# Kernel optimization log

Measured on AMD Instinct MI355X. Metric: run time of the kernel, lower is better.

## Reference

```python
import jax, jax.numpy as jnp
import numpy as np

B, S, D, H = 2, 2048, 1024, 16  # batch, seq, rep_dim, num_heads
DH = D // H
MASK_VALUE = -1e-06  # value passed by MHAttention to masked_softmax (NOT -1e6)


def setup_inputs() -> dict:
    key = jax.random.key(0)
    ks = jax.random.split(key, 16)
    def xavier(k, shape):
        fan_in, fan_out = shape[0], shape[1]
        limit = float(np.sqrt(6.0 / (fan_in + fan_out)))
        return jax.random.uniform(k, shape, jnp.float32, -limit, limit)
    return {
        "queries": jax.random.normal(ks[0], (B, S, D), jnp.float32),
        "keys": jax.random.normal(ks[1], (B, S, D), jnp.float32),
        "values": jax.random.normal(ks[2], (B, S, D), jnp.float32),
        "thresholds": jax.random.randint(ks[3], (B,), 1, S + 1, jnp.int32),
        # Linear params stored as (in, out) so y = x @ W + b
        "Wq": xavier(ks[4], (D, D)), "bq": jnp.zeros((D,), jnp.float32),
        "Wk": xavier(ks[5], (D, D)), "bk": jnp.zeros((D,), jnp.float32),
        "Wv": xavier(ks[6], (D, D)), "bv": jnp.zeros((D,), jnp.float32),
        "W": xavier(ks[7], (DH, DH)),  # learnable bilinear attention matrix
        "Wo": xavier(ks[8], (D, D)), "bo": jnp.zeros((D,), jnp.float32),
    }


def reference(queries, keys, values, thresholds, Wq, bq, Wk, bk, Wv, bv, W, Wo, bo):
    def split_heads(x):  # (B,S,D) -> (B,H,S,DH)
        return x.reshape(B, S, H, DH).transpose(0, 2, 1, 3)

    Q = split_heads(queries @ Wq + bq)
    K = split_heads(keys @ Wk + bk)
    V = split_heads(values @ Wv + bv)

    # bilinear scores: (Q @ W) @ K^T, no 1/sqrt(d) scaling in original
    scores = jnp.einsum("bhqd,bhkd->bhqk", Q @ W, K)
    # mask key positions >= threshold[b] with MASK_VALUE before softmax
    keep = jnp.arange(S)[None, None, None, :] < thresholds[:, None, None, None]
    scores = jnp.where(keep, scores, MASK_VALUE)
    attn = jax.nn.softmax(scores, axis=-1)

    out = jnp.einsum("bhqk,bhkd->bhqd", attn, V)
    out = out.transpose(0, 2, 1, 3).reshape(B, S, D)  # merge heads
    return out @ Wo + bo
```

## Files before the change

### kernel.cpp

```cpp
#include <hip/hip_runtime.h>
#include <hip/hip_bf16.h>

#define D_MODEL 1024
#define NHEADS  16
#define DH      64
#define SEQ     2048
#define BATCH   2

#define LOG2E 1.4426950408889634f
#define MASKB2 (-1e-6f * LOG2E)
#define DEFER_THR 11.5456f
#define NEG_INF (-__builtin_inff())

typedef __attribute__((ext_vector_type(8))) short short8;
typedef __attribute__((ext_vector_type(4))) short short4v;
typedef __attribute__((ext_vector_type(4))) float f32x4;

#define AS1C(p) ((const __attribute__((address_space(1))) void*)(p))
#define AS3(p)  ((__attribute__((address_space(3))) void*)(p))

union PB { short4v s4; unsigned int u[2]; };

static __device__ __forceinline__ float fexp2(float x) {
    return __builtin_amdgcn_exp2f(x);
}

static __device__ __forceinline__ unsigned int pk2(float lo, float hi) {
    __hip_bfloat16 a = __float2bfloat16(lo), b = __float2bfloat16(hi);
    unsigned short au = *(unsigned short*)&a, bu = *(unsigned short*)&b;
    return (unsigned int)au | ((unsigned int)bu << 16);
}

__global__ __launch_bounds__(256) void fold_kernel(const float* __restrict__ Wq,
                                                   const float* __restrict__ bq,
                                                   const float* __restrict__ W,
                                                   float* __restrict__ Wq2,
                                                   float* __restrict__ bq2) {
    if (blockIdx.x < 4096) {
        int idx = blockIdx.x * 256 + threadIdx.x;
        int row = idx >> 10;
        int col = idx & 1023;
        int h = col >> 6, j = col & 63;
        const float* wqr = Wq + (size_t)row * D_MODEL + h * DH;
        float s = 0.f;
#pragma unroll
        for (int d = 0; d < DH; ++d) s += wqr[d] * W[d * DH + j];
        Wq2[idx] = s * LOG2E;
    } else {
        int col = (blockIdx.x - 4096) * 256 + threadIdx.x;
        int h = col >> 6, j = col & 63;
        float s = 0.f;
#pragma unroll
        for (int d = 0; d < DH; ++d) s += bq[h * DH + d] * W[d * DH + j];
        bq2[col] = s * LOG2E;
    }
}

__global__ __launch_bounds__(256) void convert3_kernel(const float* __restrict__ q,
                                                       const float* __restrict__ k,
                                                       const float* __restrict__ v,
                                                       __hip_bfloat16* __restrict__ oq,
                                                       __hip_bfloat16* __restrict__ ok,
                                                       __hip_bfloat16* __restrict__ ov) {
    int z = blockIdx.x >> 11;
    int i = (blockIdx.x & 2047) * 256 + threadIdx.x;
    const float* in = (z == 0) ? q : (z == 1) ? k : v;
    __hip_bfloat16* out = (z == 0) ? oq : (z == 1) ? ok : ov;
    float4 a = *(const float4*)(in + (size_t)i * 8);
    float4 b = *(const float4*)(in + (size_t)i * 8 + 4);
    __hip_bfloat16 o[8];
    o[0] = __float2bfloat16(a.x); o[1] = __float2bfloat16(a.y);
    o[2] = __float2bfloat16(a.z); o[3] = __float2bfloat16(a.w);
    o[4] = __float2bfloat16(b.x); o[5] = __float2bfloat16(b.y);
    o[6] = __float2bfloat16(b.z); o[7] = __float2bfloat16(b.w);
    *(short8*)(out + (size_t)i * 8) = *(short8*)o;
}

__global__ __launch_bounds__(256) void transpose4_kernel(const float* __restrict__ W0,
                                                         const float* __restrict__ W1,
                                                         const float* __restrict__ W2,
                                                         const float* __restrict__ W3,
                                                         __hip_bfloat16* __restrict__ T0,
                                                         __hip_bfloat16* __restrict__ T1,
                                                         __hip_bfloat16* __restrict__ T2,
                                                         __hip_bfloat16* __restrict__ T3) {
    __shared__ float sT[32][33];
    int z = blockIdx.z;
    const float* Win = (z == 0) ? W0 : (z == 1) ? W1 : (z == 2) ? W2 : W3;
    __hip_bfloat16* Wt = (z == 0) ? T0 : (z == 1) ? T1 : (z == 2) ? T2 : T3;
    int n0 = blockIdx.x * 32, k0 = blockIdx.y * 32;
    int tx = threadIdx.x & 31, ty = threadIdx.x >> 5;
#pragma unroll
    for (int i = 0; i < 4; ++i)
        sT[ty + i * 8][tx] = Win[(size_t)(k0 + ty + i * 8) * D_MODEL + n0 + tx];
    __syncthreads();
#pragma unroll
    for (int i = 0; i < 4; ++i)
        Wt[(size_t)(n0 + ty + i * 8) * D_MODEL + k0 + tx] = __float2bfloat16(sT[tx][ty + i * 8]);
}

#define GEMM_CORE(A_, BT_)                                                                  \
    __shared__ __hip_bfloat16 sA[2][128 * 32];                                              \
    __shared__ __hip_bfloat16 sB[2][64 * 32];                                               \
    const int t = threadIdx.x;                                                              \
    const int lane = t & 63, w = t >> 6;                                                    \
    const int g = lane >> 4, li = lane & 15;                                                \
    const int r0 = blockIdx.y * 128, c0 = blockIdx.x * 64;                                  \
    const int wr = (w >> 1) * 64, wc = (w & 1) * 32;                                        \
    f32x4 acc[4][2] = {};                                                                   \
    auto stage = [&](int bb, int k0) {                                                      \
        _Pragma("unroll")                                                                   \
        for (int i = 0; i < 2; ++i) {                                                       \
            int o = (i * 4 + w) * 1024 + lane * 16;                                         \
            int row = o >> 6, ce = (o & 63) >> 1;                                           \
            __builtin_amdgcn_global_load_lds(AS1C(A_ + (size_t)(r0 + row) * 1024 + k0 + ce),\
                                             AS3((char*)sA[bb] + (i * 4 + w) * 1024), 16, 0, 0); \
        }                                                                                   \
        {                                                                                   \
            int o = w * 1024 + lane * 16;                                                   \
            int row = o >> 6, ce = (o & 63) >> 1;                                           \
            __builtin_amdgcn_global_load_lds(AS1C(BT_ + (size_t)(c0 + row) * 1024 + k0 + ce),\
                                             AS3((char*)sB[bb] + w * 1024), 16, 0, 0);      \
        }                                                                                   \
    };                                                                                      \
    stage(0, 0);                                                                            \
    asm volatile("s_waitcnt vmcnt(0)" ::: "memory");                                        \
    __syncthreads();                                                                        \
    int cur = 0;                                                                            \
    for (int k0 = 0; k0 < 1024; k0 += 32) {                                                 \
        if (k0 + 32 < 1024) stage(cur ^ 1, k0 + 32);                                        \
        short8 af[4], bf[2];                                                                \
        _Pragma("unroll")                                                                   \
        for (int m = 0; m < 4; ++m)                                                         \
            af[m] = *(const short8*)(sA[cur] + (wr + m * 16 + li) * 32 + g * 8);            \
        _Pragma("unroll")                                                                   \
        for (int n = 0; n < 2; ++n)                                                         \
            bf[n] = *(const short8*)(sB[cur] + (wc + n * 16 + li) * 32 + g * 8);            \
        _Pragma("unroll")                                                                   \
        for (int m = 0; m < 4; ++m)                                                         \
            _Pragma("unroll")                                                               \
            for (int n = 0; n < 2; ++n)                                                     \
                acc[m][n] = __builtin_amdgcn_mfma_f32_16x16x32_bf16(af[m], bf[n], acc[m][n], 0, 0, 0); \
        asm volatile("s_waitcnt vmcnt(0)" ::: "memory");                                    \
        __syncthreads();                                                                    \
        cur ^= 1;                                                                           \
    }

__global__ __launch_bounds__(256) void gemm_qkv_kernel(
    const __hip_bfloat16* __restrict__ Xq, const __hip_bfloat16* __restrict__ Xk,
    const __hip_bfloat16* __restrict__ Xv,
    const __hip_bfloat16* __restrict__ WqT, const __hip_bfloat16* __restrict__ WkT,
    const __hip_bfloat16* __restrict__ WvT,
    const float* __restrict__ bq2, const float* __restrict__ bk, const float* __restrict__ bv,
    __hip_bfloat16* __restrict__ Qp, __hip_bfloat16* __restrict__ Kp,
    __hip_bfloat16* __restrict__ Vt) {
    const int z = blockIdx.z;
    const __hip_bfloat16* A  = (z == 0) ? Xq  : (z == 1) ? Xk  : Xv;
    const __hip_bfloat16* BT = (z == 0) ? WqT : (z == 1) ? WkT : WvT;
    const float* bias        = (z == 0) ? bq2 : (z == 1) ? bk  : bv;
    __hip_bfloat16* C        = (z == 0) ? Qp  : (z == 1) ? Kp  : Vt;

    GEMM_CORE(A, BT)

#pragma unroll
    for (int m = 0; m < 4; ++m) {
#pragma unroll
        for (int n = 0; n < 2; ++n) {
            int col = c0 + wc + n * 16 + li;
            float bs = bias[col];
            int row0 = r0 + wr + m * 16 + g * 4;
            int h = col >> 6, d = col & 63;
            if (z == 2) {
                int b = row0 >> 11, s0 = row0 & 2047;
                __hip_bfloat16 o4[4];
#pragma unroll
                for (int r = 0; r < 4; ++r) o4[r] = __float2bfloat16(acc[m][n][r] + bs);
                *(short4*)(C + (((size_t)(b * NHEADS + h)) * DH + d) * SEQ + s0) = *(short4*)o4;
            } else {
#pragma unroll
                for (int r = 0; r < 4; ++r) {
                    int row = row0 + r;
                    int b = row >> 11, s = row & 2047;
                    C[(((size_t)(b * NHEADS + h)) * SEQ + s) * DH + d] =
                        __float2bfloat16(acc[m][n][r] + bs);
                }
            }
        }
    }
}

__global__ __launch_bounds__(256) void gemm_out_kernel(
    const __hip_bfloat16* __restrict__ A, const __hip_bfloat16* __restrict__ BT,
    const float* __restrict__ bias, float* __restrict__ C) {
    GEMM_CORE(A, BT)
#pragma unroll
    for (int m = 0; m < 4; ++m) {
#pragma unroll
        for (int n = 0; n < 2; ++n) {
            int col = c0 + wc + n * 16 + li;
            float bs = bias[col];
            int row0 = r0 + wr + m * 16 + g * 4;
#pragma unroll
            for (int r = 0; r < 4; ++r)
                C[(size_t)(row0 + r) * D_MODEL + col] = acc[m][n][r] + bs;
        }
    }
}

__global__ __launch_bounds__(256) void vsum_kernel(const __hip_bfloat16* __restrict__ Vt,
                                                   const int* __restrict__ thresholds,
                                                   float* __restrict__ Vsum) {
    int bh = blockIdx.x, b = bh >> 4;
    int thresh = thresholds[b];
    int loop_end = min(SEQ, ((thresh + 63) >> 6) << 6);
    int t = threadIdx.x;
    int dh = t >> 2, sub = t & 3;
    const __hip_bfloat16* row = Vt + ((size_t)bh * DH + dh) * SEQ;
    float s = 0.f;
    for (int s0 = loop_end + sub * 8; s0 < SEQ; s0 += 32) {
        short8 v = *(const short8*)(row + s0);
#pragma unroll
        for (int j = 0; j < 8; ++j) {
            unsigned short us = (unsigned short)v[j];
            s += __bfloat162float(*(__hip_bfloat16*)&us);
        }
    }
    s += __shfl_xor(s, 1);
    s += __shfl_xor(s, 2);
    if (sub == 0) Vsum[bh * DH + dh] = s;
}

__global__ __launch_bounds__(256) void attn_mfma_kernel(
    const __hip_bfloat16* __restrict__ Qp,
    const __hip_bfloat16* __restrict__ Kp,
    const __hip_bfloat16* __restrict__ Vt,
    const int* __restrict__ thresholds,
    const float* __restrict__ Vsum,
    __hip_bfloat16* __restrict__ AO) {
    __shared__ char lds[32768];
    char* sK  = lds;
    char* sVT = lds + 16384;

    const int t = threadIdx.x, lane = t & 63, w = t >> 6;
    const int g = lane >> 4, li = lane & 15;
    const int bh = blockIdx.x, b = bh >> 4, h = bh & 15;
    const int q0 = blockIdx.y * 128;
    const int thresh = thresholds[b];
    const int loop_end = min(SEQ, ((thresh + 63) >> 6) << 6);
    const __hip_bfloat16* Qb = Qp + (size_t)bh * SEQ * DH;
    const __hip_bfloat16* Kb = Kp + (size_t)bh * SEQ * DH;
    const __hip_bfloat16* Vb = Vt + (size_t)bh * DH * SEQ;

    short8 qf[2][2];
#pragma unroll
    for (int mq = 0; mq < 2; ++mq)
#pragma unroll
        for (int kb = 0; kb < 2; ++kb)
            qf[mq][kb] = *(const short8*)(Qb + (size_t)(q0 + w * 32 + mq * 16 + li) * DH +
                                          kb * 32 + g * 8);

    f32x4 Oacc[2][4] = {};
    float mrun[2] = {NEG_INF, NEG_INF};
    float lrun[2] = {0.f, 0.f};

    auto stageK = [&](int bb, int kv) {
#pragma unroll
        for (int i = 0; i < 2; ++i) {
            int o = i * 4096 + w * 1024 + lane * 16;
            int key = o >> 7, slot = (o & 127) >> 4;
            __builtin_amdgcn_global_load_lds(
                AS1C(Kb + (size_t)(kv + key) * DH + ((slot ^ (key & 7)) << 3)),
                AS3(sK + bb * 8192 + i * 4096 + w * 1024), 16, 0, 0);
        }
    };
    auto stageV = [&](int bb, int kv) {
#pragma unroll
        for (int i = 0; i < 2; ++i) {
            int o = i * 4096 + w * 1024 + lane * 16;
            int dh = o >> 7, slot = (o & 127) >> 4;
            __builtin_amdgcn_global_load_lds(
                AS1C(Vb + (size_t)dh * SEQ + kv + ((slot ^ (dh & 7)) << 3)),
                AS3(sVT + bb * 8192 + i * 4096 + w * 1024), 16, 0, 0);
        }
    };

    stageK(0, 0); stageV(0, 0);
    asm volatile("s_waitcnt vmcnt(0)" ::: "memory");
    __syncthreads();

    int cur = 0;
    for (int kv0 = 0; kv0 < loop_end; kv0 += 64) {
        int nxt = kv0 + 64;
        if (nxt < loop_end) { stageK(cur ^ 1, nxt); stageV(cur ^ 1, nxt); }

        f32x4 S[2][4] = {};
        __builtin_amdgcn_s_setprio(1);
#pragma unroll
        for (int kb = 0; kb < 2; ++kb) {
            short8 kf[4];
#pragma unroll
            for (int n = 0; n < 4; ++n) {
                int key = 16 * n + li;
                kf[n] = *(const short8*)(sK + cur * 8192 + key * 128 +
                                         (((4 * kb + g) ^ (key & 7)) << 4));
            }
#pragma unroll
            for (int mq = 0; mq < 2; ++mq)
#pragma unroll
                for (int n = 0; n < 4; ++n)
                    S[mq][n] = __builtin_amdgcn_mfma_f32_16x16x32_bf16(kf[n], qf[mq][kb],
                                                                       S[mq][n], 0, 0, 0);
        }
        __builtin_amdgcn_s_setprio(0);

        if (kv0 + 64 > thresh) {
            int tr = thresh - kv0 - 4 * g;
#pragma unroll
            for (int n = 0; n < 4; ++n)
#pragma unroll
                for (int rr = 0; rr < 4; ++rr)
                    if (16 * n + rr >= tr) { S[0][n][rr] = MASKB2; S[1][n][rr] = MASKB2; }
        }

        float pmax[2];
#pragma unroll
        for (int mq = 0; mq < 2; ++mq) {
            float mx = S[mq][0][0];
#pragma unroll
            for (int n = 0; n < 4; ++n)
#pragma unroll
                for (int rr = 0; rr < 4; ++rr) mx = fmaxf(mx, S[mq][n][rr]);
            mx = fmaxf(mx, __shfl_xor(mx, 16));
            mx = fmaxf(mx, __shfl_xor(mx, 32));
            pmax[mq] = mx;
        }

        bool need = (pmax[0] > mrun[0] + DEFER_THR) || (pmax[1] > mrun[1] + DEFER_THR);
        if (__any(need)) {
#pragma unroll
            for (int mq = 0; mq < 2; ++mq) {
                float mn = fmaxf(mrun[mq], pmax[mq]);
                float alpha = fexp2(mrun[mq] - mn);
                lrun[mq] *= alpha;
#pragma unroll
                for (int n = 0; n < 4; ++n)
#pragma unroll
                    for (int rr = 0; rr < 4; ++rr) Oacc[mq][n][rr] *= alpha;
                mrun[mq] = mn;
            }
        }

        short4v pb[2][4];
#pragma unroll
        for (int mq = 0; mq < 2; ++mq) {
            float rs = 0.f;
#pragma unroll
            for (int n = 0; n < 4; ++n) {
#pragma unroll
                for (int rr = 0; rr < 4; ++rr) {
                    float p = fexp2(S[mq][n][rr] - mrun[mq]);
                    S[mq][n][rr] = p;
                    rs += p;
                }
                PB u;
                u.u[0] = pk2(S[mq][n][0], S[mq][n][1]);
                u.u[1] = pk2(S[mq][n][2], S[mq][n][3]);
                pb[mq][n] = u.s4;
            }
            rs += __shfl_xor(rs, 16);
            rs += __shfl_xor(rs, 32);
            lrun[mq] += rs;
        }

        __builtin_amdgcn_s_setprio(1);
#pragma unroll
        for (int ks = 0; ks < 4; ++ks) {
            int slot = 2 * ks + (g >> 1);
            int sub8 = 8 * (g & 1);
#pragma unroll
            for (int n = 0; n < 4; ++n) {
                int dh = 16 * n + li;
                short4v va = *(const short4v*)(sVT + cur * 8192 + dh * 128 +
                                               ((slot ^ (dh & 7)) << 4) + sub8);
#pragma unroll
                for (int mq = 0; mq < 2; ++mq)
                    Oacc[mq][n] = __builtin_amdgcn_mfma_f32_16x16x16bf16_1k(va, pb[mq][ks],
                                                                            Oacc[mq][n], 0, 0, 0);
            }
        }
        __builtin_amdgcn_s_setprio(0);

        asm volatile("s_waitcnt vmcnt(0)" ::: "memory");
        __syncthreads();
        cur ^= 1;
    }

    int nmask = SEQ - loop_end;
    if (nmask > 0) {
        const float* vs = Vsum + bh * DH;
        f32x4 vsf[4];
#pragma unroll
        for (int n = 0; n < 4; ++n) vsf[n] = *(const f32x4*)(vs + 16 * n + 4 * g);
#pragma unroll
        for (int mq = 0; mq < 2; ++mq) {
            float pu = fexp2(MASKB2 - mrun[mq]);
            lrun[mq] += (float)nmask * pu;
#pragma unroll
            for (int n = 0; n < 4; ++n)
#pragma unroll
                for (int rr = 0; rr < 4; ++rr) Oacc[mq][n][rr] += pu * vsf[n][rr];
        }
    }

#pragma unroll
    for (int mq = 0; mq < 2; ++mq) {
        float linv = 1.0f / lrun[mq];
        int q = q0 + w * 32 + mq * 16 + li;
#pragma unroll
        for (int n = 0; n < 4; ++n) {
            __hip_bfloat16 o4[4];
#pragma unroll
            for (int rr = 0; rr < 4; ++rr) o4[rr] = __float2bfloat16(Oacc[mq][n][rr] * linv);
            *(short4*)(AO + (size_t)(b * SEQ + q) * D_MODEL + h * DH + 16 * n + 4 * g) =
                *(short4*)o4;
        }
    }
}

extern "C" void kernel_launch(void* const* d_in, const int* in_sizes, int n_in,
                              void* d_out, int out_size, void* d_ws, size_t ws_size,
                              hipStream_t stream) {
    const float* queries    = (const float*)d_in[0];
    const float* keys       = (const float*)d_in[1];
    const float* values     = (const float*)d_in[2];
    const int*   thresholds = (const int*)d_in[3];
    const float* Wq = (const float*)d_in[4];
    const float* bq = (const float*)d_in[5];
    const float* Wk = (const float*)d_in[6];
    const float* bk = (const float*)d_in[7];
    const float* Wv = (const float*)d_in[8];
    const float* bv = (const float*)d_in[9];
    const float* W  = (const float*)d_in[10];
    const float* Wo = (const float*)d_in[11];
    const float* bo = (const float*)d_in[12];
    float* out = (float*)d_out;

    char* wsb = (char*)d_ws;
    float* bq2  = (float*)wsb;
    float* Vsum = (float*)(wsb + 4096);
    float* Wq2  = (float*)(wsb + 16384);
    __hip_bfloat16* XqB = (__hip_bfloat16*)(wsb + 16384 + (4 << 20));
    __hip_bfloat16* XkB = XqB + (1 << 22);
    __hip_bfloat16* XvB = XkB + (1 << 22);
    __hip_bfloat16* WqT = XvB + (1 << 22);
    __hip_bfloat16* WkT = WqT + (1 << 20);
    __hip_bfloat16* WvT = WkT + (1 << 20);
    __hip_bfloat16* WoT = WvT + (1 << 20);
    __hip_bfloat16* QpB = WoT + (1 << 20);
    __hip_bfloat16* KpB = QpB + (1 << 22);
    __hip_bfloat16* VtB = KpB + (1 << 22);
    __hip_bfloat16* AOB = XqB;

    fold_kernel<<<4100, 256, 0, stream>>>(Wq, bq, W, Wq2, bq2);
    convert3_kernel<<<6144, 256, 0, stream>>>(queries, keys, values, XqB, XkB, XvB);
    transpose4_kernel<<<dim3(32, 32, 4), 256, 0, stream>>>(Wq2, Wk, Wv, Wo,
                                                           WqT, WkT, WvT, WoT);

    gemm_qkv_kernel<<<dim3(16, 32, 3), 256, 0, stream>>>(XqB, XkB, XvB, WqT, WkT, WvT,
                                                         bq2, bk, bv, QpB, KpB, VtB);
    vsum_kernel<<<32, 256, 0, stream>>>(VtB, thresholds, Vsum);

    attn_mfma_kernel<<<dim3(32, 16), 256, 0, stream>>>(QpB, KpB, VtB, thresholds, Vsum, AOB);

    gemm_out_kernel<<<dim3(16, 32), 256, 0, stream>>>(AOB, WoT, bo, out);
}
```

Baseline: 181.6 us.

## Drop LDS staging in attention; load K/V directly from global per wave

The attention kernel now runs one wave per block (64 threads, 2048 blocks) instead of four waves sharing double-buffered, swizzled K/V tiles in LDS. Each wave reads its K and V fragments straight from global memory, which removes the LDS staging, the barriers and the waitcnt syncs. The cost is that K/V reuse across the four waves now has to come from the L2/L1 cache, and the V reads are narrow 8-byte strided accesses. The row-max reduction is also rewritten as a balanced tree.

```diff
diff --git a/kernel.cpp b/kernel.cpp
--- a/kernel.cpp
+++ b/kernel.cpp
@@ -230,21 +230,17 @@
     if (sub == 0) Vsum[bh * DH + dh] = s;
 }
 
-__global__ __launch_bounds__(256) void attn_mfma_kernel(
+__global__ __launch_bounds__(64) void attn_mfma_kernel(
     const __hip_bfloat16* __restrict__ Qp,
     const __hip_bfloat16* __restrict__ Kp,
     const __hip_bfloat16* __restrict__ Vt,
     const int* __restrict__ thresholds,
     const float* __restrict__ Vsum,
     __hip_bfloat16* __restrict__ AO) {
-    __shared__ char lds[32768];
-    char* sK  = lds;
-    char* sVT = lds + 16384;
-
-    const int t = threadIdx.x, lane = t & 63, w = t >> 6;
+    const int lane = threadIdx.x;
     const int g = lane >> 4, li = lane & 15;
     const int bh = blockIdx.x, b = bh >> 4, h = bh & 15;
-    const int q0 = blockIdx.y * 128;
+    const int q0 = blockIdx.y * 32;
     const int thresh = thresholds[b];
     const int loop_end = min(SEQ, ((thresh + 63) >> 6) << 6);
     const __hip_bfloat16* Qb = Qp + (size_t)bh * SEQ * DH;
@@ -256,61 +252,32 @@
     for (int mq = 0; mq < 2; ++mq)
 #pragma unroll
         for (int kb = 0; kb < 2; ++kb)
-            qf[mq][kb] = *(const short8*)(Qb + (size_t)(q0 + w * 32 + mq * 16 + li) * DH +
+            qf[mq][kb] = *(const short8*)(Qb + (size_t)(q0 + mq * 16 + li) * DH +
                                           kb * 32 + g * 8);
 
     f32x4 Oacc[2][4] = {};
     float mrun[2] = {NEG_INF, NEG_INF};
     float lrun[2] = {0.f, 0.f};
 
-    auto stageK = [&](int bb, int kv) {
-#pragma unroll
-        for (int i = 0; i < 2; ++i) {
-            int o = i * 4096 + w * 1024 + lane * 16;
-            int key = o >> 7, slot = (o & 127) >> 4;
-            __builtin_amdgcn_global_load_lds(
-                AS1C(Kb + (size_t)(kv + key) * DH + ((slot ^ (key & 7)) << 3)),
-                AS3(sK + bb * 8192 + i * 4096 + w * 1024), 16, 0, 0);
-        }
-    };
-    auto stageV = [&](int bb, int kv) {
-#pragma unroll
-        for (int i = 0; i < 2; ++i) {
-            int o = i * 4096 + w * 1024 + lane * 16;
-            int dh = o >> 7, slot = (o & 127) >> 4;
-            __builtin_amdgcn_global_load_lds(
-                AS1C(Vb + (size_t)dh * SEQ + kv + ((slot ^ (dh & 7)) << 3)),
-                AS3(sVT + bb * 8192 + i * 4096 + w * 1024), 16, 0, 0);
-        }
-    };
-
-    stageK(0, 0); stageV(0, 0);
-    asm volatile("s_waitcnt vmcnt(0)" ::: "memory");
-    __syncthreads();
-
-    int cur = 0;
     for (int kv0 = 0; kv0 < loop_end; kv0 += 64) {
-        int nxt = kv0 + 64;
-        if (nxt < loop_end) { stageK(cur ^ 1, nxt); stageV(cur ^ 1, nxt); }
+        short8 kf[2][4];
+#pragma unroll
+        for (int kb = 0; kb < 2; ++kb)
+#pragma unroll
+            for (int n = 0; n < 4; ++n)
+                kf[kb][n] = *(const short8*)(Kb + (size_t)(kv0 + 16 * n + li) * DH +
+                                             kb * 32 + g * 8);
 
         f32x4 S[2][4] = {};
         __builtin_amdgcn_s_setprio(1);
 #pragma unroll
-        for (int kb = 0; kb < 2; ++kb) {
-            short8 kf[4];
-#pragma unroll
-            for (int n = 0; n < 4; ++n) {
-                int key = 16 * n + li;
-                kf[n] = *(const short8*)(sK + cur * 8192 + key * 128 +
-                                         (((4 * kb + g) ^ (key & 7)) << 4));
-            }
+        for (int kb = 0; kb < 2; ++kb)
 #pragma unroll
             for (int mq = 0; mq < 2; ++mq)
 #pragma unroll
                 for (int n = 0; n < 4; ++n)
-                    S[mq][n] = __builtin_amdgcn_mfma_f32_16x16x32_bf16(kf[n], qf[mq][kb],
+                    S[mq][n] = __builtin_amdgcn_mfma_f32_16x16x32_bf16(kf[kb][n], qf[mq][kb],
                                                                        S[mq][n], 0, 0, 0);
-        }
         __builtin_amdgcn_s_setprio(0);
 
         if (kv0 + 64 > thresh) {
@@ -325,11 +292,11 @@
         float pmax[2];
 #pragma unroll
         for (int mq = 0; mq < 2; ++mq) {
-            float mx = S[mq][0][0];
-#pragma unroll
-            for (int n = 0; n < 4; ++n)
-#pragma unroll
-                for (int rr = 0; rr < 4; ++rr) mx = fmaxf(mx, S[mq][n][rr]);
+            float a0 = fmaxf(fmaxf(S[mq][0][0], S[mq][0][1]), fmaxf(S[mq][0][2], S[mq][0][3]));
+            float a1 = fmaxf(fmaxf(S[mq][1][0], S[mq][1][1]), fmaxf(S[mq][1][2], S[mq][1][3]));
+            float a2 = fmaxf(fmaxf(S[mq][2][0], S[mq][2][1]), fmaxf(S[mq][2][2], S[mq][2][3]));
+            float a3 = fmaxf(fmaxf(S[mq][3][0], S[mq][3][1]), fmaxf(S[mq][3][2], S[mq][3][3]));
+            float mx = fmaxf(fmaxf(a0, a1), fmaxf(a2, a3));
             mx = fmaxf(mx, __shfl_xor(mx, 16));
             mx = fmaxf(mx, __shfl_xor(mx, 32));
             pmax[mq] = mx;
@@ -375,13 +342,10 @@
         __builtin_amdgcn_s_setprio(1);
 #pragma unroll
         for (int ks = 0; ks < 4; ++ks) {
-            int slot = 2 * ks + (g >> 1);
-            int sub8 = 8 * (g & 1);
+            int soff = kv0 + 16 * ks + 4 * g;
 #pragma unroll
             for (int n = 0; n < 4; ++n) {
-                int dh = 16 * n + li;
-                short4v va = *(const short4v*)(sVT + cur * 8192 + dh * 128 +
-                                               ((slot ^ (dh & 7)) << 4) + sub8);
+                short4v va = *(const short4v*)(Vb + (size_t)(16 * n + li) * SEQ + soff);
 #pragma unroll
                 for (int mq = 0; mq < 2; ++mq)
                     Oacc[mq][n] = __builtin_amdgcn_mfma_f32_16x16x16bf16_1k(va, pb[mq][ks],
@@ -389,10 +353,6 @@
             }
         }
         __builtin_amdgcn_s_setprio(0);
-
-        asm volatile("s_waitcnt vmcnt(0)" ::: "memory");
-        __syncthreads();
-        cur ^= 1;
     }
 
     int nmask = SEQ - loop_end;
@@ -415,7 +375,7 @@
 #pragma unroll
     for (int mq = 0; mq < 2; ++mq) {
         float linv = 1.0f / lrun[mq];
-        int q = q0 + w * 32 + mq * 16 + li;
+        int q = q0 + mq * 16 + li;
 #pragma unroll
         for (int n = 0; n < 4; ++n) {
             __hip_bfloat16 o4[4];
@@ -470,7 +430,7 @@
                                                          bq2, bk, bv, QpB, KpB, VtB);
     vsum_kernel<<<32, 256, 0, stream>>>(VtB, thresholds, Vsum);
 
-    attn_mfma_kernel<<<dim3(32, 16), 256, 0, stream>>>(QpB, KpB, VtB, thresholds, Vsum, AOB);
+    attn_mfma_kernel<<<dim3(32, 64), 64, 0, stream>>>(QpB, KpB, VtB, thresholds, Vsum, AOB);
 
     gemm_out_kernel<<<dim3(16, 32), 256, 0, stream>>>(AOB, WoT, bo, out);
 }
```

Result: slower. 260.7 us (+43.6%).
